# Kernel optimization log

Hardware: AMD Instinct MI355X
Metric: run time of the kernel (lower is better)

## Reference

```python
import jax, jax.numpy as jnp
import numpy as np

N_EMBED = 384
NUM_EXPERTS = 8
TOP_K = 2


def setup_inputs() -> dict:
    key = jax.random.key(0)
    k_x, k_n, k_w1, k_b1, k_w2, k_b2 = jax.random.split(key, 6)
    B, T = 16, 4096
    bound = 1.0 / np.sqrt(N_EMBED)
    return {
        "x": jax.random.normal(k_x, (B, T, N_EMBED), dtype=jnp.float32),
        "noise": jax.random.normal(k_n, (B, T, NUM_EXPERTS), dtype=jnp.float32),
        "w_route": jax.random.uniform(k_w1, (NUM_EXPERTS, N_EMBED), jnp.float32, -bound, bound),
        "b_route": jax.random.uniform(k_b1, (NUM_EXPERTS,), jnp.float32, -bound, bound),
        "w_noise": jax.random.uniform(k_w2, (NUM_EXPERTS, N_EMBED), jnp.float32, -bound, bound),
        "b_noise": jax.random.uniform(k_b2, (NUM_EXPERTS,), jnp.float32, -bound, bound),
    }


def reference(x, noise, w_route, b_route, w_noise, b_noise):
    # two tiny linears: [B,T,D] @ [D,E] -> [B,T,E]
    logits = jnp.einsum("btd,ed->bte", x, w_route) + b_route
    noise_logits = jnp.einsum("btd,ed->bte", x, w_noise) + b_noise
    noisy_logits = logits + noise * jax.nn.softplus(noise_logits)

    top_k_logits, indices = jax.lax.top_k(noisy_logits, TOP_K)  # [B,T,k]

    # scatter top-k values into a -inf tensor; equivalently mask non-topk to -inf
    # (values at the top-k positions are exactly the noisy logits there)
    mask = jax.nn.one_hot(indices, NUM_EXPERTS, dtype=jnp.bool_).any(axis=-2)  # [B,T,E]
    sparse_logits = jnp.where(mask, noisy_logits, -jnp.inf)
    router_output = jax.nn.softmax(sparse_logits, axis=-1)
    return router_output, indices
```

## Files before the change

kernel.cpp:

```cpp
#include <hip/hip_runtime.h>
#include <math.h>


constexpr int D = 384;

__device__ __forceinline__ float dpp_xor1(float v) {
    return __int_as_float(__builtin_amdgcn_update_dpp(
        0, __float_as_int(v), 0xB1, 0xF, 0xF, true));
}
__device__ __forceinline__ float dpp_xor2(float v) {
    return __int_as_float(__builtin_amdgcn_update_dpp(
        0, __float_as_int(v), 0x4E, 0xF, 0xF, true));
}
__device__ __forceinline__ float swz_xor4(float v) {
    return __int_as_float(__builtin_amdgcn_ds_swizzle(__float_as_int(v), 0x101F));
}
__device__ __forceinline__ float swz_xor8(float v) {
    return __int_as_float(__builtin_amdgcn_ds_swizzle(__float_as_int(v), 0x201F));
}
__device__ __forceinline__ float swz_xor16(float v) {
    return __int_as_float(__builtin_amdgcn_ds_swizzle(__float_as_int(v), 0x401F));
}

__global__ __launch_bounds__(256, 4) void noisy_topk_router_f32(
    const float* __restrict__ x,
    const float* __restrict__ noise,
    const float* __restrict__ w_route,
    const float* __restrict__ b_route,
    const float* __restrict__ w_noise,
    const float* __restrict__ b_noise,
    float* __restrict__ out,
    int ntok)
{
    __shared__ float w_lds[16 * D];
    __shared__ float bias[16];

    const int tid = threadIdx.x;

#pragma unroll
    for (int r = 0; r < 3; ++r) {
        int i = (tid + 256 * r) * 4;
        *(float4*)(w_lds + i)        = *(const float4*)(w_route + i);
        *(float4*)(w_lds + 3072 + i) = *(const float4*)(w_noise + i);
    }
    if (tid < 8)       bias[tid] = b_route[tid];
    else if (tid < 16) bias[tid] = b_noise[tid - 8];
    __syncthreads();

    const int wave = tid >> 6;
    const int lane = tid & 63;
    const int p    = lane & 1;
    const int c    = (lane >> 1) & 15;
    const int g    = lane >> 5;
    const int tok0 = blockIdx.x * 32 + wave * 8 + g * 4;

    float acc[4][8];
#pragma unroll
    for (int t = 0; t < 4; ++t)
#pragma unroll
        for (int e = 0; e < 8; ++e) acc[t][e] = 0.f;

    const float* xr = x + (size_t)tok0 * D + c * 4;
    const float* wb = w_lds + (p * 8) * D + c * 4;

    float4 xa[4], xn[4];
#pragma unroll
    for (int t = 0; t < 4; ++t) xa[t] = *(const float4*)(xr + t * D);

#pragma unroll
    for (int j = 0; j < 6; ++j) {
        const int jn = (j < 5) ? (j + 1) * 64 : 0;
#pragma unroll
        for (int t = 0; t < 4; ++t) xn[t] = *(const float4*)(xr + t * D + jn);

        const float* wj = wb + j * 64;
#pragma unroll
        for (int e = 0; e < 8; ++e) {
            float4 wv = *(const float4*)(wj + e * D);
            acc[0][e] += xa[0].x * wv.x + xa[0].y * wv.y + xa[0].z * wv.z + xa[0].w * wv.w;
            acc[1][e] += xa[1].x * wv.x + xa[1].y * wv.y + xa[1].z * wv.z + xa[1].w * wv.w;
            acc[2][e] += xa[2].x * wv.x + xa[2].y * wv.y + xa[2].z * wv.z + xa[2].w * wv.w;
            acc[3][e] += xa[3].x * wv.x + xa[3].y * wv.y + xa[3].z * wv.z + xa[3].w * wv.w;
        }
#pragma unroll
        for (int t = 0; t < 4; ++t) xa[t] = xn[t];
    }

    const bool b0 = (c & 1), b1 = (c >> 1) & 1;
    float a2[2][8];
#pragma unroll
    for (int u = 0; u < 2; ++u)
#pragma unroll
        for (int e = 0; e < 8; ++e) {
            float s = b0 ? acc[2 * u][e]     : acc[2 * u + 1][e];
            float k = b0 ? acc[2 * u + 1][e] : acc[2 * u][e];
            a2[u][e] = k + dpp_xor2(s);
        }
    float a1[8];
#pragma unroll
    for (int e = 0; e < 8; ++e) {
        float s = b1 ? a2[0][e] : a2[1][e];
        float k = b1 ? a2[1][e] : a2[0][e];
        a1[e] = k + swz_xor4(s);
    }
#pragma unroll
    for (int e = 0; e < 8; ++e) a1[e] += swz_xor8(a1[e]);
#pragma unroll
    for (int e = 0; e < 8; ++e) a1[e] += swz_xor16(a1[e]);

    float oth[8];
#pragma unroll
    for (int e = 0; e < 8; ++e) oth[e] = dpp_xor1(a1[e]);

    if (p == 0 && c < 4) {
        const int token = tok0 + c;
        float4 n0 = *(const float4*)(noise + (size_t)token * 8);
        float4 n1 = *(const float4*)(noise + (size_t)token * 8 + 4);
        float nz[8] = {n0.x, n0.y, n0.z, n0.w, n1.x, n1.y, n1.z, n1.w};

        float noisy[8];
#pragma unroll
        for (int e = 0; e < 8; ++e) {
            float lg = a1[e]  + bias[e];
            float nl = oth[e] + bias[8 + e];
            float sp = fmaxf(nl, 0.f) + log1pf(expf(-fabsf(nl)));
            noisy[e] = lg + nz[e] * sp;
        }

        float v0 = noisy[0]; int i0 = 0;
#pragma unroll
        for (int e = 1; e < 8; ++e)
            if (noisy[e] > v0) { v0 = noisy[e]; i0 = e; }
        float v1 = -INFINITY; int i1 = 0;
#pragma unroll
        for (int e = 0; e < 8; ++e)
            if (e != i0 && noisy[e] > v1) { v1 = noisy[e]; i1 = e; }

        float ex  = expf(v1 - v0);
        float inv = 1.f / (1.f + ex);
        float p0  = inv;
        float p1  = ex * inv;

        float pr[8];
#pragma unroll
        for (int e = 0; e < 8; ++e)
            pr[e] = (e == i0) ? p0 : ((e == i1) ? p1 : 0.f);

        float* orow = out + (size_t)token * 8;
        *(float4*)(orow)     = make_float4(pr[0], pr[1], pr[2], pr[3]);
        *(float4*)(orow + 4) = make_float4(pr[4], pr[5], pr[6], pr[7]);

        *(float2*)(out + (size_t)ntok * 8 + (size_t)token * 2) =
            make_float2((float)i0, (float)i1);
    }
}

extern "C" void kernel_launch(void* const* d_in, const int* in_sizes, int n_in,
                              void* d_out, int out_size, void* d_ws, size_t ws_size,
                              hipStream_t stream) {
    const float* x       = (const float*)d_in[0];
    const float* noise   = (const float*)d_in[1];
    const float* w_route = (const float*)d_in[2];
    const float* b_route = (const float*)d_in[3];
    const float* w_noise = (const float*)d_in[4];
    const float* b_noise = (const float*)d_in[5];
    float* out = (float*)d_out;

    const int ntok   = in_sizes[0] / D;
    const int blocks = ntok / 32;

    hipLaunchKernelGGL(noisy_topk_router_f32, dim3(blocks), dim3(256), 0, stream,
                       x, noise, w_route, b_route, w_noise, b_noise, out, ntok);
}
```

Measured before the change: 165.6 us.

## Stage token tile in LDS and interleave padded weights, halve tokens per block

Each block now copies its 16 tokens of x into shared memory and reads them from LDS, replacing the per-thread global loads with software prefetch. Route and noise weights are interleaved row-wise with a padded stride to change the LDS bank pattern, and the block handles 16 tokens (2 per thread group) instead of 32, with one fewer reduction stage. This doubles the grid and raises LDS use per block, with occupancy hint lowered to 3, and adds a full sync before compute, so global loads no longer overlap with math.

```diff
diff --git a/kernel.cpp b/kernel.cpp
--- a/kernel.cpp
+++ b/kernel.cpp
@@ -3,6 +3,8 @@
 
 
 constexpr int D = 384;
+constexpr int TPB = 16;
+constexpr int WS = 388;
 
 __device__ __forceinline__ float dpp_xor1(float v) {
     return __int_as_float(__builtin_amdgcn_update_dpp(
@@ -22,7 +24,7 @@
     return __int_as_float(__builtin_amdgcn_ds_swizzle(__float_as_int(v), 0x401F));
 }
 
-__global__ __launch_bounds__(256, 4) void noisy_topk_router_f32(
+__global__ __launch_bounds__(256, 3) void noisy_topk_router_f32(
     const float* __restrict__ x,
     const float* __restrict__ noise,
     const float* __restrict__ w_route,
@@ -32,77 +34,67 @@
     float* __restrict__ out,
     int ntok)
 {
-    __shared__ float w_lds[16 * D];
+    __shared__ float x_tile[TPB * D];
+    __shared__ float w_lds[16 * WS];
     __shared__ float bias[16];
 
-    const int tid = threadIdx.x;
+    const int tid  = threadIdx.x;
+    const int tok0 = blockIdx.x * TPB;
 
+    const float* xg = x + (size_t)tok0 * D;
 #pragma unroll
-    for (int r = 0; r < 3; ++r) {
-        int i = (tid + 256 * r) * 4;
-        *(float4*)(w_lds + i)        = *(const float4*)(w_route + i);
-        *(float4*)(w_lds + 3072 + i) = *(const float4*)(w_noise + i);
+    for (int i = 0; i < 6; ++i) {
+        const int f = (tid + i * 256) * 4;
+        *(float4*)(x_tile + f) = *(const float4*)(xg + f);
+    }
+#pragma unroll
+    for (int i = 0; i < 3; ++i) {
+        const int f = (tid + i * 256) * 4;
+        const int e = f / 384, d = f - e * 384;
+        *(float4*)(w_lds + (2 * e)     * WS + d) = *(const float4*)(w_route + f);
+        *(float4*)(w_lds + (2 * e + 1) * WS + d) = *(const float4*)(w_noise + f);
     }
     if (tid < 8)       bias[tid] = b_route[tid];
     else if (tid < 16) bias[tid] = b_noise[tid - 8];
     __syncthreads();
 
-    const int wave = tid >> 6;
-    const int lane = tid & 63;
-    const int p    = lane & 1;
-    const int c    = (lane >> 1) & 15;
-    const int g    = lane >> 5;
-    const int tok0 = blockIdx.x * 32 + wave * 8 + g * 4;
+    const int p = tid & 1;
+    const int c = (tid >> 1) & 15;
+    const int g = tid >> 5;
 
-    float acc[4][8];
+    float acc[2][8];
 #pragma unroll
-    for (int t = 0; t < 4; ++t)
+    for (int t = 0; t < 2; ++t)
 #pragma unroll
         for (int e = 0; e < 8; ++e) acc[t][e] = 0.f;
 
-    const float* xr = x + (size_t)tok0 * D + c * 4;
-    const float* wb = w_lds + (p * 8) * D + c * 4;
-
-    float4 xa[4], xn[4];
-#pragma unroll
-    for (int t = 0; t < 4; ++t) xa[t] = *(const float4*)(xr + t * D);
+    const float* xt0 = x_tile + (g * 2) * D;
+    const float* xt1 = x_tile + (g * 2 + 1) * D;
+    const float* wb  = w_lds + p * WS;
 
 #pragma unroll
     for (int j = 0; j < 6; ++j) {
-        const int jn = (j < 5) ? (j + 1) * 64 : 0;
-#pragma unroll
-        for (int t = 0; t < 4; ++t) xn[t] = *(const float4*)(xr + t * D + jn);
-
-        const float* wj = wb + j * 64;
+        const int dof = j * 64 + c * 4;
+        float4 x0 = *(const float4*)(xt0 + dof);
+        float4 x1 = *(const float4*)(xt1 + dof);
 #pragma unroll
         for (int e = 0; e < 8; ++e) {
-            float4 wv = *(const float4*)(wj + e * D);
-            acc[0][e] += xa[0].x * wv.x + xa[0].y * wv.y + xa[0].z * wv.z + xa[0].w * wv.w;
-            acc[1][e] += xa[1].x * wv.x + xa[1].y * wv.y + xa[1].z * wv.z + xa[1].w * wv.w;
-            acc[2][e] += xa[2].x * wv.x + xa[2].y * wv.y + xa[2].z * wv.z + xa[2].w * wv.w;
-            acc[3][e] += xa[3].x * wv.x + xa[3].y * wv.y + xa[3].z * wv.z + xa[3].w * wv.w;
+            float4 wv = *(const float4*)(wb + e * 2 * WS + dof);
+            acc[0][e] += x0.x * wv.x + x0.y * wv.y + x0.z * wv.z + x0.w * wv.w;
+            acc[1][e] += x1.x * wv.x + x1.y * wv.y + x1.z * wv.z + x1.w * wv.w;
         }
-#pragma unroll
-        for (int t = 0; t < 4; ++t) xa[t] = xn[t];
     }
 
-    const bool b0 = (c & 1), b1 = (c >> 1) & 1;
-    float a2[2][8];
-#pragma unroll
-    for (int u = 0; u < 2; ++u)
-#pragma unroll
-        for (int e = 0; e < 8; ++e) {
-            float s = b0 ? acc[2 * u][e]     : acc[2 * u + 1][e];
-            float k = b0 ? acc[2 * u + 1][e] : acc[2 * u][e];
-            a2[u][e] = k + dpp_xor2(s);
-        }
+    const bool b0 = (c & 1);
     float a1[8];
 #pragma unroll
     for (int e = 0; e < 8; ++e) {
-        float s = b1 ? a2[0][e] : a2[1][e];
-        float k = b1 ? a2[1][e] : a2[0][e];
-        a1[e] = k + swz_xor4(s);
+        float s = b0 ? acc[0][e] : acc[1][e];
+        float k = b0 ? acc[1][e] : acc[0][e];
+        a1[e] = k + dpp_xor2(s);
     }
+#pragma unroll
+    for (int e = 0; e < 8; ++e) a1[e] += swz_xor4(a1[e]);
 #pragma unroll
     for (int e = 0; e < 8; ++e) a1[e] += swz_xor8(a1[e]);
 #pragma unroll
@@ -112,8 +104,8 @@
 #pragma unroll
     for (int e = 0; e < 8; ++e) oth[e] = dpp_xor1(a1[e]);
 
-    if (p == 0 && c < 4) {
-        const int token = tok0 + c;
+    if (p == 0 && c < 2) {
+        const int token = tok0 + g * 2 + c;
         float4 n0 = *(const float4*)(noise + (size_t)token * 8);
         float4 n1 = *(const float4*)(noise + (size_t)token * 8 + 4);
         float nz[8] = {n0.x, n0.y, n0.z, n0.w, n1.x, n1.y, n1.z, n1.w};
@@ -167,7 +159,7 @@
     float* out = (float*)d_out;
 
     const int ntok   = in_sizes[0] / D;
-    const int blocks = ntok / 32;
+    const int blocks = ntok / TPB;
 
     hipLaunchKernelGGL(noisy_topk_router_f32, dim3(blocks), dim3(256), 0, stream,
                        x, noise, w_route, b_route, w_noise, b_noise, out, ntok);
```

Measured after the change: 175.7 us. 6.1% more time.
